# Optimization experiments

Hardware: AMD Instinct MI355X
Metric: run time of the kernel (lower is better)

Reference implementation:

```python
import jax, jax.numpy as jnp
import numpy as np

EMBED_DIM = 1024
NUM_HEADS = 16
PROJ_DIM = EMBED_DIM // NUM_HEADS


def setup_inputs() -> dict:
    key = jax.random.key(0)
    ks = jax.random.split(key, 11)
    B, S, D = 2, 2048, EMBED_DIM
    scale = 1.0 / np.sqrt(D)
    inp = {
        'q': jax.random.normal(ks[0], (B, S, D), jnp.float32),
        'k': jax.random.normal(ks[1], (B, S, D), jnp.float32),
        'v': jax.random.normal(ks[2], (B, S, D), jnp.float32),
        'Wq': jax.random.normal(ks[3], (D, D), jnp.float32) * scale,
        'bq': jnp.zeros((D,), jnp.float32),
        'Wk': jax.random.normal(ks[4], (D, D), jnp.float32) * scale,
        'bk': jnp.zeros((D,), jnp.float32),
        'Wv': jax.random.normal(ks[5], (D, D), jnp.float32) * scale,
        'bv': jnp.zeros((D,), jnp.float32),
        'Wo': jax.random.normal(ks[6], (D, D), jnp.float32) * scale,
        'bo': jnp.zeros((D,), jnp.float32),
        'use_causal_mask': 1,
    }
    return inp


def _split_heads(x, B):
    # [B, S, D] -> [B, H, S, Pd]
    return x.reshape(B, -1, NUM_HEADS, PROJ_DIM).transpose(0, 2, 1, 3)


def reference(q, k, v, Wq, bq, Wk, bk, Wv, bv, Wo, bo, use_causal_mask):
    B, S, D = q.shape
    qh = _split_heads(q @ Wq + bq, B)
    kh = _split_heads(k @ Wk + bk, B)
    vh = _split_heads(v @ Wv + bv, B)
    # scaled dot-product attention; scores [B, H, S, S]
    logits = jnp.einsum('bhqd,bhkd->bhqk', qh, kh) / jnp.sqrt(
        jnp.asarray(PROJ_DIM, jnp.float32))
    if use_causal_mask:
        # faithful to source: logits += log(tril * 1e-9 + 1e-9)
        tril = jnp.tril(jnp.ones((S, S), dtype=logits.dtype))
        logits = logits + jnp.log(tril * 1e-9 + 1e-9)
    attn = jax.nn.softmax(logits, axis=-1)
    out = jnp.einsum('bhqk,bhkd->bhqd', attn, vh)
    out = out.transpose(0, 2, 1, 3).reshape(B, S, D)
    return out @ Wo + bo
```

## Files before the change

### kernel.cpp

```cpp
#include <hip/hip_runtime.h>
#include <hip/hip_bf16.h>
#include <stdint.h>

#define EMBED 1024
#define NH    16
#define PD    64
#define BATCH 2
#define SEQ   2048

typedef unsigned short u16;
typedef __attribute__((ext_vector_type(8))) short bf16x8;
typedef __attribute__((ext_vector_type(4))) float f32x4;

#define WAITALL() __builtin_amdgcn_s_waitcnt(0)

__device__ __forceinline__ float b2f(u16 x) {
  unsigned u = ((unsigned)x) << 16;
  return __builtin_bit_cast(float, u);
}
__device__ __forceinline__ u16 cvtb(float x) {
  __bf16 h = (__bf16)x;
  return __builtin_bit_cast(u16, h);
}
__device__ __forceinline__ float loadIn(const void* p, size_t i, int isf32) {
  return isf32 ? ((const float*)p)[i] : b2f(((const u16*)p)[i]);
}
__device__ __forceinline__ void async16(const void* g, void* l) {
  __builtin_amdgcn_global_load_lds((const __attribute__((address_space(1))) void*)g,
                                   (__attribute__((address_space(3))) void*)l,
                                   16, 0, 0);
}

__global__ void detect(const unsigned* q, int* flag) {
  int lane = threadIdx.x;
  unsigned lo = q[lane] & 0xffffu;
  unsigned e = (lo >> 7) & 0xffu;
  int pred = (e >= 110 && e <= 135);
  unsigned long long m = __ballot(pred);
  if (lane == 0) flag[0] = (__popcll(m) < 32) ? 1 : 0;
}

__global__ __launch_bounds__(256) void conv_qkv(const void* q, const void* k,
                                                const void* v, u16* qb, u16* kb,
                                                u16* vb, const int* flag) {
  const int isf32 = flag[0];
  size_t i = ((size_t)blockIdx.x * 256 + threadIdx.x) * 8;
  const void* src = (blockIdx.y == 0) ? q : (blockIdx.y == 1) ? k : v;
  u16* dst = (blockIdx.y == 0) ? qb : (blockIdx.y == 1) ? kb : vb;
  u16 tmp[8];
  if (isf32) {
    const float* s = (const float*)src + i;
    float4 a = *(const float4*)s;
    float4 b = *(const float4*)(s + 4);
    tmp[0] = cvtb(a.x); tmp[1] = cvtb(a.y); tmp[2] = cvtb(a.z); tmp[3] = cvtb(a.w);
    tmp[4] = cvtb(b.x); tmp[5] = cvtb(b.y); tmp[6] = cvtb(b.z); tmp[7] = cvtb(b.w);
  } else {
    const uint4 r = *(const uint4*)((const u16*)src + i);
    *(uint4*)tmp = r;
  }
  *(uint4*)(dst + i) = *(uint4*)tmp;
}

__global__ __launch_bounds__(256) void conv_w(const void* Wq, const void* Wk,
                                              const void* Wv, const void* Wo,
                                              u16* out, const int* flag) {
  const int isf32 = flag[0];
  const void* W = (blockIdx.z == 0) ? Wq : (blockIdx.z == 1) ? Wk
                : (blockIdx.z == 2) ? Wv : Wo;
  u16* WT = out + (size_t)blockIdx.z * EMBED * EMBED;
  __shared__ float sh[64][65];
  int r0 = blockIdx.y * 64, c0 = blockIdx.x * 64;
  int col = threadIdx.x & 63;
  int rb  = threadIdx.x >> 6;
#pragma unroll
  for (int i = 0; i < 16; i++) {
    int row = i * 4 + rb;
    sh[row][col] = loadIn(W, (size_t)(r0 + row) * EMBED + c0 + col, isf32);
  }
  __syncthreads();
#pragma unroll
  for (int i = 0; i < 16; i++) {
    int row = i * 4 + rb;
    WT[(size_t)(c0 + row) * EMBED + r0 + col] = cvtb(sh[col][row]);
  }
}

__device__ __forceinline__ void gemm_stage(const u16* __restrict__ A,
                                           const u16* __restrict__ Bt,
                                           int tm, int tn, int kt,
                                           u16* As, u16* Bs, int tid) {
#pragma unroll
  for (int i = 0; i < 4; i++) {
    int c = i * 256 + tid;
    int row = c >> 3;
    int col = ((c & 7) << 3) ^ ((row & 7) << 3);
    async16(A + (size_t)(tm + row) * EMBED + kt + col, As + c * 8);
    async16(Bt + (size_t)(tn + row) * EMBED + kt + col, Bs + c * 8);
  }
}

__device__ __forceinline__ void gemm_compute(const u16* As, const u16* Bs,
                                             int wm, int wn, int l15, int quad,
                                             int rbx, f32x4 acc[4][4]) {
#pragma unroll
  for (int ks = 0; ks < 64; ks += 32) {
    int ko = (ks + quad * 8) ^ rbx;
    bf16x8 af[4], bf[4];
#pragma unroll
    for (int mt = 0; mt < 4; mt++)
      af[mt] = *(const bf16x8*)(As + (wm + mt * 16 + l15) * 64 + ko);
#pragma unroll
    for (int nt = 0; nt < 4; nt++)
      bf[nt] = *(const bf16x8*)(Bs + (wn + nt * 16 + l15) * 64 + ko);
#pragma unroll
    for (int mt = 0; mt < 4; mt++)
#pragma unroll
      for (int nt = 0; nt < 4; nt++)
        acc[mt][nt] = __builtin_amdgcn_mfma_f32_16x16x32_bf16(
            af[mt], bf[nt], acc[mt][nt], 0, 0, 0);
  }
}

__global__ __launch_bounds__(256) void qkv_gemm(
    const u16* qb, const u16* kb, const u16* vb, const u16* wts,
    const void* bq, const void* bk, const void* bv,
    u16* Qh, u16* Kh, u16* Vt, const int* flag) {
  __shared__ __align__(16) u16 lds[2 * 128 * 64];
  const int isf32 = flag[0];
  int z = blockIdx.z;
  const u16* A = (z == 0) ? qb : (z == 1) ? kb : vb;
  const u16* Bt = wts + (size_t)z * EMBED * EMBED;
  const void* bias = (z == 0) ? bq : (z == 1) ? bk : bv;
  int tm = blockIdx.y * 128, tn = blockIdx.x * 128;

  const int tid = threadIdx.x, lane = tid & 63, wv = tid >> 6;
  const int wm = (wv >> 1) * 64, wn = (wv & 1) * 64;
  const int l15 = lane & 15, quad = lane >> 4;
  const int rbx = (lane & 7) << 3;
  f32x4 acc[4][4];
  f32x4 zz = {0.f, 0.f, 0.f, 0.f};
#pragma unroll
  for (int i = 0; i < 4; i++)
#pragma unroll
    for (int j = 0; j < 4; j++) acc[i][j] = zz;

  for (int kt = 0; kt < EMBED; kt += 64) {
    gemm_stage(A, Bt, tm, tn, kt, lds, lds + 8192, tid);
    WAITALL();
    __syncthreads();
    gemm_compute(lds, lds + 8192, wm, wn, l15, quad, rbx, acc);
    __syncthreads();
  }

  int rbase = tm + wm + (quad << 2);
  int cbase = tn + wn + l15;
  if (z < 2) {
    u16* dst = (z == 0) ? Qh : Kh;
#pragma unroll
    for (int mt = 0; mt < 4; mt++)
#pragma unroll
      for (int nt = 0; nt < 4; nt++) {
        int col = cbase + nt * 16;
        float bv_ = loadIn(bias, col, isf32);
        int h = col >> 6, p = col & 63;
#pragma unroll
        for (int j = 0; j < 4; j++) {
          int row = rbase + mt * 16 + j;
          int b = row >> 11, s = row & 2047;
          dst[(((size_t)(b * NH + h) * SEQ) + s) * PD + p] =
              cvtb(acc[mt][nt][j] + bv_);
        }
      }
  } else {
#pragma unroll
    for (int mt = 0; mt < 4; mt++)
#pragma unroll
      for (int nt = 0; nt < 4; nt++) {
        int col = cbase + nt * 16;
        float bv_ = loadIn(bias, col, isf32);
        int h = col >> 6, p = col & 63;
        int row0 = rbase + mt * 16;
        int b = row0 >> 11, s0 = row0 & 2047;
        int beta = s0 >> 5, w = s0 & 31;
        int pos = (beta << 5) + (((w >> 2) & 3) << 3) + ((w >> 4) << 2);
        ushort4 pk;
        pk.x = cvtb(acc[mt][nt][0] + bv_);
        pk.y = cvtb(acc[mt][nt][1] + bv_);
        pk.z = cvtb(acc[mt][nt][2] + bv_);
        pk.w = cvtb(acc[mt][nt][3] + bv_);
        *(ushort4*)(Vt + ((size_t)(b * NH + h) * PD + p) * SEQ + pos) = pk;
      }
  }
}

__global__ __launch_bounds__(256) void attn(const u16* __restrict__ Qh,
                                            const u16* __restrict__ Kh,
                                            const u16* __restrict__ Vt,
                                            u16* __restrict__ O,
                                            const int* __restrict__ maskflag) {
  __shared__ __align__(16) u16 Qs[128 * 64];
  __shared__ __align__(16) u16 Ks[2][64 * 64];
  __shared__ __align__(16) u16 Vs[2][64 * 64];
  const int bh = blockIdx.y;
  const int qt = blockIdx.x * 128;
  const int tid = threadIdx.x, lane = tid & 63, wv = tid >> 6;
  const int l15 = lane & 15, quad = lane >> 4;
  const int rbx = (lane & 7) << 3;
  const size_t head = (size_t)bh * SEQ * PD;
  const bool causal = (maskflag[0] != 0);
  const float C = 0.18033688011112042f;

  const int c0 = tid, c1 = 256 + tid;
  const int r0 = c0 >> 3, r1 = c1 >> 3;
  const int x0 = ((c0 & 7) << 3) ^ ((r0 & 7) << 3);
  const int x1 = ((c1 & 7) << 3) ^ ((r1 & 7) << 3);

#pragma unroll
  for (int i = 0; i < 4; i++) {
    int c = i * 256 + tid;
    int row = c >> 3;
    int col = ((c & 7) << 3) ^ ((row & 7) << 3);
    async16(Qh + head + (size_t)(qt + row) * PD + col, Qs + c * 8);
  }
  async16(Kh + head + (size_t)r0 * PD + x0, Ks[0] + c0 * 8);
  async16(Kh + head + (size_t)r1 * PD + x1, Ks[0] + c1 * 8);
  async16(Vt + head + (size_t)r0 * SEQ + x0, Vs[0] + c0 * 8);
  async16(Vt + head + (size_t)r1 * SEQ + x1, Vs[0] + c1 * 8);
  WAITALL();
  __syncthreads();

  bf16x8 qf[2][2];
#pragma unroll
  for (int ks = 0; ks < 2; ks++) {
    int ko = (ks * 32 + quad * 8) ^ rbx;
    qf[ks][0] = *(const bf16x8*)(Qs + (wv * 32 + l15) * 64 + ko);
    qf[ks][1] = *(const bf16x8*)(Qs + (wv * 32 + 16 + l15) * 64 + ko);
  }

  float lacc[2] = {0.f, 0.f};
  f32x4 oacc[4][2];
  f32x4 z4 = {0.f, 0.f, 0.f, 0.f};
#pragma unroll
  for (int mt = 0; mt < 4; mt++)
#pragma unroll
    for (int n = 0; n < 2; n++) oacc[mt][n] = z4;

  const int rowq = qt + wv * 32;

  for (int t = 0; t < SEQ / 64; t++) {
    const int k0 = t * 64;
    const int cur = t & 1;
    if (t + 1 < SEQ / 64) {
      const int kn = k0 + 64;
      u16* Kn = Ks[cur ^ 1];
      u16* Vn = Vs[cur ^ 1];
      async16(Kh + head + (size_t)(kn + r0) * PD + x0, Kn + c0 * 8);
      async16(Kh + head + (size_t)(kn + r1) * PD + x1, Kn + c1 * 8);
      async16(Vt + head + (size_t)r0 * SEQ + kn + x0, Vn + c0 * 8);
      async16(Vt + head + (size_t)r1 * SEQ + kn + x1, Vn + c1 * 8);
    }
    const u16* Ksc = Ks[cur];
    const u16* Vsc = Vs[cur];

    f32x4 st[4][2];
#pragma unroll
    for (int kt = 0; kt < 4; kt++)
#pragma unroll
      for (int n = 0; n < 2; n++) st[kt][n] = z4;
#pragma unroll
    for (int ks = 0; ks < 2; ks++) {
      int ko = (ks * 32 + quad * 8) ^ rbx;
#pragma unroll
      for (int kt = 0; kt < 4; kt++) {
        bf16x8 kf = *(const bf16x8*)(Ksc + (kt * 16 + l15) * 64 + ko);
        st[kt][0] = __builtin_amdgcn_mfma_f32_16x16x32_bf16(kf, qf[ks][0], st[kt][0], 0, 0, 0);
        st[kt][1] = __builtin_amdgcn_mfma_f32_16x16x32_bf16(kf, qf[ks][1], st[kt][1], 0, 0, 0);
      }
    }

    const int mode = !causal ? 0 : (k0 > qt + 127 ? 2 : (k0 + 63 <= qt ? 0 : 1));
    const float ub = (mode == 2) ? -17.f : -16.f;
    unsigned pw[2][2][4];
#pragma unroll
    for (int kt = 0; kt < 4; kt++) {
#pragma unroll
      for (int n = 0; n < 2; n++) {
        const int qrow = rowq + n * 16 + l15;
        float p[4];
#pragma unroll
        for (int r = 0; r < 4; r++) {
          float bias = ub;
          if (mode == 1) {
            int kappa = k0 + kt * 16 + 4 * quad + r;
            bias = (kappa > qrow) ? -17.f : -16.f;
          }
          p[r] = exp2f(fmaf(st[kt][n][r], C, bias));
        }
        lacc[n] += (p[0] + p[1]) + (p[2] + p[3]);
        pw[kt >> 1][n][(kt & 1) * 2 + 0] =
            (unsigned)cvtb(p[0]) | ((unsigned)cvtb(p[1]) << 16);
        pw[kt >> 1][n][(kt & 1) * 2 + 1] =
            (unsigned)cvtb(p[2]) | ((unsigned)cvtb(p[3]) << 16);
      }
    }

#pragma unroll
    for (int p = 0; p < 2; p++) {
      bf16x8 pf[2];
      pf[0] = __builtin_bit_cast(bf16x8,
          (uint4){pw[p][0][0], pw[p][0][1], pw[p][0][2], pw[p][0][3]});
      pf[1] = __builtin_bit_cast(bf16x8,
          (uint4){pw[p][1][0], pw[p][1][1], pw[p][1][2], pw[p][1][3]});
#pragma unroll
      for (int mt = 0; mt < 4; mt++) {
        int row = mt * 16 + l15;
        int chunk = ((p << 2) + quad) ^ (row & 7);
        bf16x8 vf = *(const bf16x8*)(Vsc + row * 64 + (chunk << 3));
        oacc[mt][0] = __builtin_amdgcn_mfma_f32_16x16x32_bf16(vf, pf[0], oacc[mt][0], 0, 0, 0);
        oacc[mt][1] = __builtin_amdgcn_mfma_f32_16x16x32_bf16(vf, pf[1], oacc[mt][1], 0, 0, 0);
      }
    }
    WAITALL();
    __syncthreads();
  }

#pragma unroll
  for (int n = 0; n < 2; n++) {
    lacc[n] += __shfl_xor(lacc[n], 16, 64);
    lacc[n] += __shfl_xor(lacc[n], 32, 64);
  }
  float inv[2] = {1.f / lacc[0], 1.f / lacc[1]};

  const int b = bh >> 4, h = bh & 15;
#pragma unroll
  for (int mt = 0; mt < 4; mt++) {
#pragma unroll
    for (int n = 0; n < 2; n++) {
      int qrow = rowq + n * 16 + l15;
      ushort4 w;
      w.x = cvtb(oacc[mt][n][0] * inv[n]);
      w.y = cvtb(oacc[mt][n][1] * inv[n]);
      w.z = cvtb(oacc[mt][n][2] * inv[n]);
      w.w = cvtb(oacc[mt][n][3] * inv[n]);
      *(ushort4*)(O + ((size_t)b * SEQ + qrow) * EMBED + h * PD + mt * 16 +
                  4 * quad) = w;
    }
  }
}

__global__ __launch_bounds__(256) void out_gemm(const u16* __restrict__ Ob,
                                                const u16* __restrict__ WoT,
                                                const void* __restrict__ bo,
                                                void* __restrict__ out,
                                                const int* __restrict__ flag) {
  __shared__ __align__(16) u16 lds[4 * 128 * 64];
  const int isf32 = flag[0];
  int tm = blockIdx.y * 128, tn = blockIdx.x * 128;
  const int tid = threadIdx.x, lane = tid & 63, wv = tid >> 6;
  const int wm = (wv >> 1) * 64, wn = (wv & 1) * 64;
  const int l15 = lane & 15, quad = lane >> 4;
  const int rbx = (lane & 7) << 3;
  f32x4 acc[4][4];
  f32x4 zz = {0.f, 0.f, 0.f, 0.f};
#pragma unroll
  for (int i = 0; i < 4; i++)
#pragma unroll
    for (int j = 0; j < 4; j++) acc[i][j] = zz;

  gemm_stage(Ob, WoT, tm, tn, 0, lds, lds + 8192, tid);
  WAITALL();
  __syncthreads();
  for (int kt = 0; kt < EMBED; kt += 64) {
    const int cur = (kt >> 6) & 1;
    u16* curb = lds + cur * 16384;
    if (kt + 64 < EMBED)
      gemm_stage(Ob, WoT, tm, tn, kt + 64, lds + (cur ^ 1) * 16384,
                 lds + (cur ^ 1) * 16384 + 8192, tid);
    gemm_compute(curb, curb + 8192, wm, wn, l15, quad, rbx, acc);
    WAITALL();
    __syncthreads();
  }

  int rbase = tm + wm + (quad << 2);
  int cbase = tn + wn + l15;
#pragma unroll
  for (int mt = 0; mt < 4; mt++)
#pragma unroll
    for (int nt = 0; nt < 4; nt++) {
      int col = cbase + nt * 16;
      float bv_ = loadIn(bo, col, isf32);
#pragma unroll
      for (int j = 0; j < 4; j++) {
        int row = rbase + mt * 16 + j;
        float val = acc[mt][nt][j] + bv_;
        size_t off = (size_t)row * EMBED + col;
        if (isf32) ((float*)out)[off] = val;
        else       ((u16*)out)[off]   = cvtb(val);
      }
    }
}

extern "C" void kernel_launch(void* const* d_in, const int* in_sizes, int n_in,
                              void* d_out, int out_size, void* d_ws, size_t ws_size,
                              hipStream_t stream) {
  const void* q  = d_in[0];
  const void* k  = d_in[1];
  const void* v  = d_in[2];
  const void* Wq = d_in[3];
  const void* bq = d_in[4];
  const void* Wk = d_in[5];
  const void* bk = d_in[6];
  const void* Wv = d_in[7];
  const void* bv = d_in[8];
  const void* Wo = d_in[9];
  const void* bo = d_in[10];
  const int* msk = (const int*)d_in[11];

  char* ws = (char*)d_ws;
  int*  flag  = (int*)ws;
  u16*  qb    = (u16*)(ws + 64);
  u16*  kb    = qb + (size_t)4194304;
  u16*  vb    = kb + (size_t)4194304;
  u16*  WT    = vb + (size_t)4194304;
  u16*  Qh    = WT + (size_t)4194304;
  u16*  Kh    = Qh + (size_t)4194304;
  u16*  Vt    = Kh + (size_t)4194304;
  u16*  Ob    = Vt + (size_t)4194304;

  detect<<<1, 64, 0, stream>>>((const unsigned*)q, flag);
  conv_qkv<<<dim3(2048, 3), 256, 0, stream>>>(q, k, v, qb, kb, vb, flag);
  conv_w<<<dim3(16, 16, 4), 256, 0, stream>>>(Wq, Wk, Wv, Wo, WT, flag);
  qkv_gemm<<<dim3(8, 32, 3), 256, 0, stream>>>(qb, kb, vb, WT, bq, bk, bv,
                                               Qh, Kh, Vt, flag);
  attn<<<dim3(16, 32), 256, 0, stream>>>(Qh, Kh, Vt, Ob, msk);
  out_gemm<<<dim3(8, 32), 256, 0, stream>>>(Ob, WT + (size_t)3 * 1048576,
                                            bo, d_out, flag);
}
```

Before: 299.7 us.

## Halve attention query tile, alias Q into K buffer, fold dtype detect into conversion

The attention kernel now processes 64 query rows per block instead of 128, with each wave handling 16 rows. The Q tile is staged in the second K buffer so shared memory shrinks to 32KB, and launch bounds request 4 blocks per CU, doubling the grid for better occupancy and load balance. MFMA sections are wrapped in s_setprio to favour matrix issue. The separate dtype-detect kernel is removed by recomputing the flag inside conv_qkv. In exchange, every K/V tile is loaded twice as often per query row, which raises global and LDS traffic.

```diff
diff --git a/kernel.cpp b/kernel.cpp
--- a/kernel.cpp
+++ b/kernel.cpp
@@ -31,19 +31,16 @@
                                    16, 0, 0);
 }
 
-__global__ void detect(const unsigned* q, int* flag) {
-  int lane = threadIdx.x;
-  unsigned lo = q[lane] & 0xffffu;
-  unsigned e = (lo >> 7) & 0xffu;
+__global__ __launch_bounds__(256) void conv_qkv(const void* q, const void* k,
+                                                const void* v, u16* qb, u16* kb,
+                                                u16* vb, int* flag) {
+  unsigned w0 = ((const unsigned*)q)[threadIdx.x & 63];
+  unsigned e = (w0 >> 7) & 0xffu;
   int pred = (e >= 110 && e <= 135);
   unsigned long long m = __ballot(pred);
-  if (lane == 0) flag[0] = (__popcll(m) < 32) ? 1 : 0;
-}
-
-__global__ __launch_bounds__(256) void conv_qkv(const void* q, const void* k,
-                                                const void* v, u16* qb, u16* kb,
-                                                u16* vb, const int* flag) {
-  const int isf32 = flag[0];
+  const int isf32 = (__popcll(m) < 32) ? 1 : 0;
+  if (blockIdx.x == 0 && blockIdx.y == 0 && threadIdx.x == 0) flag[0] = isf32;
+
   size_t i = ((size_t)blockIdx.x * 256 + threadIdx.x) * 8;
   const void* src = (blockIdx.y == 0) ? q : (blockIdx.y == 1) ? k : v;
   u16* dst = (blockIdx.y == 0) ? qb : (blockIdx.y == 1) ? kb : vb;
@@ -193,16 +190,19 @@
   }
 }
 
-__global__ __launch_bounds__(256) void attn(const u16* __restrict__ Qh,
-                                            const u16* __restrict__ Kh,
-                                            const u16* __restrict__ Vt,
-                                            u16* __restrict__ O,
-                                            const int* __restrict__ maskflag) {
-  __shared__ __align__(16) u16 Qs[128 * 64];
-  __shared__ __align__(16) u16 Ks[2][64 * 64];
-  __shared__ __align__(16) u16 Vs[2][64 * 64];
+__global__ __launch_bounds__(256, 4) void attn(const u16* __restrict__ Qh,
+                                               const u16* __restrict__ Kh,
+                                               const u16* __restrict__ Vt,
+                                               u16* __restrict__ O,
+                                               const int* __restrict__ maskflag) {
+  __shared__ __align__(16) u16 sh[4 * 64 * 64];
+  u16* const Ksb0 = sh;
+  u16* const Ksb1 = sh + 4096;
+  u16* const Vsb0 = sh + 8192;
+  u16* const Vsb1 = sh + 12288;
+  u16* const Qs   = Ksb1;
   const int bh = blockIdx.y;
-  const int qt = blockIdx.x * 128;
+  const int qt = blockIdx.x * 64;
   const int tid = threadIdx.x, lane = tid & 63, wv = tid >> 6;
   const int l15 = lane & 15, quad = lane >> 4;
   const int rbx = (lane & 7) << 3;
@@ -215,136 +215,116 @@
   const int x0 = ((c0 & 7) << 3) ^ ((r0 & 7) << 3);
   const int x1 = ((c1 & 7) << 3) ^ ((r1 & 7) << 3);
 
-#pragma unroll
-  for (int i = 0; i < 4; i++) {
-    int c = i * 256 + tid;
-    int row = c >> 3;
-    int col = ((c & 7) << 3) ^ ((row & 7) << 3);
-    async16(Qh + head + (size_t)(qt + row) * PD + col, Qs + c * 8);
-  }
-  async16(Kh + head + (size_t)r0 * PD + x0, Ks[0] + c0 * 8);
-  async16(Kh + head + (size_t)r1 * PD + x1, Ks[0] + c1 * 8);
-  async16(Vt + head + (size_t)r0 * SEQ + x0, Vs[0] + c0 * 8);
-  async16(Vt + head + (size_t)r1 * SEQ + x1, Vs[0] + c1 * 8);
+  async16(Qh + head + (size_t)(qt + r0) * PD + x0, Qs + c0 * 8);
+  async16(Qh + head + (size_t)(qt + r1) * PD + x1, Qs + c1 * 8);
+  async16(Kh + head + (size_t)r0 * PD + x0, Ksb0 + c0 * 8);
+  async16(Kh + head + (size_t)r1 * PD + x1, Ksb0 + c1 * 8);
+  async16(Vt + head + (size_t)r0 * SEQ + x0, Vsb0 + c0 * 8);
+  async16(Vt + head + (size_t)r1 * SEQ + x1, Vsb0 + c1 * 8);
   WAITALL();
   __syncthreads();
 
-  bf16x8 qf[2][2];
+  bf16x8 qf[2];
 #pragma unroll
   for (int ks = 0; ks < 2; ks++) {
     int ko = (ks * 32 + quad * 8) ^ rbx;
-    qf[ks][0] = *(const bf16x8*)(Qs + (wv * 32 + l15) * 64 + ko);
-    qf[ks][1] = *(const bf16x8*)(Qs + (wv * 32 + 16 + l15) * 64 + ko);
-  }
-
-  float lacc[2] = {0.f, 0.f};
-  f32x4 oacc[4][2];
+    qf[ks] = *(const bf16x8*)(Qs + (wv * 16 + l15) * 64 + ko);
+  }
+  __syncthreads();
+
+  float lacc = 0.f;
+  f32x4 oacc[4];
   f32x4 z4 = {0.f, 0.f, 0.f, 0.f};
 #pragma unroll
-  for (int mt = 0; mt < 4; mt++)
-#pragma unroll
-    for (int n = 0; n < 2; n++) oacc[mt][n] = z4;
-
-  const int rowq = qt + wv * 32;
+  for (int mt = 0; mt < 4; mt++) oacc[mt] = z4;
+
+  const int rowq = qt + wv * 16;
+  const int qrow = rowq + l15;
 
   for (int t = 0; t < SEQ / 64; t++) {
     const int k0 = t * 64;
     const int cur = t & 1;
     if (t + 1 < SEQ / 64) {
       const int kn = k0 + 64;
-      u16* Kn = Ks[cur ^ 1];
-      u16* Vn = Vs[cur ^ 1];
+      u16* Kn = cur ? Ksb0 : Ksb1;
+      u16* Vn = cur ? Vsb0 : Vsb1;
       async16(Kh + head + (size_t)(kn + r0) * PD + x0, Kn + c0 * 8);
       async16(Kh + head + (size_t)(kn + r1) * PD + x1, Kn + c1 * 8);
       async16(Vt + head + (size_t)r0 * SEQ + kn + x0, Vn + c0 * 8);
       async16(Vt + head + (size_t)r1 * SEQ + kn + x1, Vn + c1 * 8);
     }
-    const u16* Ksc = Ks[cur];
-    const u16* Vsc = Vs[cur];
-
-    f32x4 st[4][2];
-#pragma unroll
-    for (int kt = 0; kt < 4; kt++)
-#pragma unroll
-      for (int n = 0; n < 2; n++) st[kt][n] = z4;
+    const u16* Ksc = cur ? Ksb1 : Ksb0;
+    const u16* Vsc = cur ? Vsb1 : Vsb0;
+
+    f32x4 st[4];
+#pragma unroll
+    for (int kt = 0; kt < 4; kt++) st[kt] = z4;
+    __builtin_amdgcn_s_setprio(1);
 #pragma unroll
     for (int ks = 0; ks < 2; ks++) {
       int ko = (ks * 32 + quad * 8) ^ rbx;
 #pragma unroll
       for (int kt = 0; kt < 4; kt++) {
         bf16x8 kf = *(const bf16x8*)(Ksc + (kt * 16 + l15) * 64 + ko);
-        st[kt][0] = __builtin_amdgcn_mfma_f32_16x16x32_bf16(kf, qf[ks][0], st[kt][0], 0, 0, 0);
-        st[kt][1] = __builtin_amdgcn_mfma_f32_16x16x32_bf16(kf, qf[ks][1], st[kt][1], 0, 0, 0);
+        st[kt] = __builtin_amdgcn_mfma_f32_16x16x32_bf16(kf, qf[ks], st[kt], 0, 0, 0);
       }
     }
-
-    const int mode = !causal ? 0 : (k0 > qt + 127 ? 2 : (k0 + 63 <= qt ? 0 : 1));
+    __builtin_amdgcn_s_setprio(0);
+
+    const int mode = !causal ? 0 : (k0 > qt + 63 ? 2 : (k0 + 63 <= qt ? 0 : 1));
     const float ub = (mode == 2) ? -17.f : -16.f;
-    unsigned pw[2][2][4];
+    unsigned pw[2][4];
 #pragma unroll
     for (int kt = 0; kt < 4; kt++) {
-#pragma unroll
-      for (int n = 0; n < 2; n++) {
-        const int qrow = rowq + n * 16 + l15;
-        float p[4];
-#pragma unroll
-        for (int r = 0; r < 4; r++) {
-          float bias = ub;
-          if (mode == 1) {
-            int kappa = k0 + kt * 16 + 4 * quad + r;
-            bias = (kappa > qrow) ? -17.f : -16.f;
-          }
-          p[r] = exp2f(fmaf(st[kt][n][r], C, bias));
+      float p[4];
+#pragma unroll
+      for (int r = 0; r < 4; r++) {
+        float bias = ub;
+        if (mode == 1) {
+          int kappa = k0 + kt * 16 + 4 * quad + r;
+          bias = (kappa > qrow) ? -17.f : -16.f;
         }
-        lacc[n] += (p[0] + p[1]) + (p[2] + p[3]);
-        pw[kt >> 1][n][(kt & 1) * 2 + 0] =
-            (unsigned)cvtb(p[0]) | ((unsigned)cvtb(p[1]) << 16);
-        pw[kt >> 1][n][(kt & 1) * 2 + 1] =
-            (unsigned)cvtb(p[2]) | ((unsigned)cvtb(p[3]) << 16);
-      }
+        p[r] = exp2f(fmaf(st[kt][r], C, bias));
+      }
+      lacc += (p[0] + p[1]) + (p[2] + p[3]);
+      pw[kt >> 1][(kt & 1) * 2 + 0] =
+          (unsigned)cvtb(p[0]) | ((unsigned)cvtb(p[1]) << 16);
+      pw[kt >> 1][(kt & 1) * 2 + 1] =
+          (unsigned)cvtb(p[2]) | ((unsigned)cvtb(p[3]) << 16);
     }
 
+    __builtin_amdgcn_s_setprio(1);
 #pragma unroll
     for (int p = 0; p < 2; p++) {
-      bf16x8 pf[2];
-      pf[0] = __builtin_bit_cast(bf16x8,
-          (uint4){pw[p][0][0], pw[p][0][1], pw[p][0][2], pw[p][0][3]});
-      pf[1] = __builtin_bit_cast(bf16x8,
-          (uint4){pw[p][1][0], pw[p][1][1], pw[p][1][2], pw[p][1][3]});
+      bf16x8 pf = __builtin_bit_cast(bf16x8,
+          (uint4){pw[p][0], pw[p][1], pw[p][2], pw[p][3]});
 #pragma unroll
       for (int mt = 0; mt < 4; mt++) {
         int row = mt * 16 + l15;
         int chunk = ((p << 2) + quad) ^ (row & 7);
         bf16x8 vf = *(const bf16x8*)(Vsc + row * 64 + (chunk << 3));
-        oacc[mt][0] = __builtin_amdgcn_mfma_f32_16x16x32_bf16(vf, pf[0], oacc[mt][0], 0, 0, 0);
-        oacc[mt][1] = __builtin_amdgcn_mfma_f32_16x16x32_bf16(vf, pf[1], oacc[mt][1], 0, 0, 0);
+        oacc[mt] = __builtin_amdgcn_mfma_f32_16x16x32_bf16(vf, pf, oacc[mt], 0, 0, 0);
       }
     }
+    __builtin_amdgcn_s_setprio(0);
     WAITALL();
     __syncthreads();
   }
 
-#pragma unroll
-  for (int n = 0; n < 2; n++) {
-    lacc[n] += __shfl_xor(lacc[n], 16, 64);
-    lacc[n] += __shfl_xor(lacc[n], 32, 64);
-  }
-  float inv[2] = {1.f / lacc[0], 1.f / lacc[1]};
+  lacc += __shfl_xor(lacc, 16, 64);
+  lacc += __shfl_xor(lacc, 32, 64);
+  float inv = 1.f / lacc;
 
   const int b = bh >> 4, h = bh & 15;
 #pragma unroll
   for (int mt = 0; mt < 4; mt++) {
-#pragma unroll
-    for (int n = 0; n < 2; n++) {
-      int qrow = rowq + n * 16 + l15;
-      ushort4 w;
-      w.x = cvtb(oacc[mt][n][0] * inv[n]);
-      w.y = cvtb(oacc[mt][n][1] * inv[n]);
-      w.z = cvtb(oacc[mt][n][2] * inv[n]);
-      w.w = cvtb(oacc[mt][n][3] * inv[n]);
-      *(ushort4*)(O + ((size_t)b * SEQ + qrow) * EMBED + h * PD + mt * 16 +
-                  4 * quad) = w;
-    }
+    ushort4 w;
+    w.x = cvtb(oacc[mt][0] * inv);
+    w.y = cvtb(oacc[mt][1] * inv);
+    w.z = cvtb(oacc[mt][2] * inv);
+    w.w = cvtb(oacc[mt][3] * inv);
+    *(ushort4*)(O + ((size_t)b * SEQ + qrow) * EMBED + h * PD + mt * 16 +
+                4 * quad) = w;
   }
 }
 
@@ -427,12 +407,11 @@
   u16*  Vt    = Kh + (size_t)4194304;
   u16*  Ob    = Vt + (size_t)4194304;
 
-  detect<<<1, 64, 0, stream>>>((const unsigned*)q, flag);
   conv_qkv<<<dim3(2048, 3), 256, 0, stream>>>(q, k, v, qb, kb, vb, flag);
   conv_w<<<dim3(16, 16, 4), 256, 0, stream>>>(Wq, Wk, Wv, Wo, WT, flag);
   qkv_gemm<<<dim3(8, 32, 3), 256, 0, stream>>>(qb, kb, vb, WT, bq, bk, bv,
                                                Qh, Kh, Vt, flag);
-  attn<<<dim3(16, 32), 256, 0, stream>>>(Qh, Kh, Vt, Ob, msk);
+  attn<<<dim3(32, 32), 256, 0, stream>>>(Qh, Kh, Vt, Ob, msk);
   out_gemm<<<dim3(8, 32), 256, 0, stream>>>(Ob, WT + (size_t)3 * 1048576,
                                             bo, d_out, flag);
 }
```

After: 281.2 us. 1.07x faster.
